# Kernel optimization log

Hardware: AMD Instinct MI355X
Metric: run time of the kernel (lower is better)

Reference implementation:

```python
import jax, jax.numpy as jnp
import numpy as np

B, S, H, R, F, E, K = 4, 2048, 1024, 256, 4096, 8, 2


def setup_inputs() -> dict:
    key = jax.random.key(0)
    k = jax.random.split(key, 7)
    s = 0.02
    return {
        "x": jax.random.normal(k[0], (B, S, H), dtype=jnp.float32),
        "router_w": jax.random.normal(k[1], (H, E), dtype=jnp.float32) * s,
        "router_b": jnp.zeros((E,), dtype=jnp.float32),
        "w1": jax.random.normal(k[2], (E, H, R), dtype=jnp.float32) * s,  # expert Linear(hidden->rank), no bias
        "w2": jax.random.normal(k[3], (E, R, F), dtype=jnp.float32) * s,  # expert Linear(rank->ffn), no bias
        "lin2_w": jax.random.normal(k[4], (F, H), dtype=jnp.float32) * s,
        "lin2_b": jnp.zeros((H,), dtype=jnp.float32),
    }


def reference(x, router_w, router_b, w1, w2, lin2_w, lin2_b):
    # Router: softmax over experts, top-k selection (mask), weight by softmax prob
    logits = jnp.einsum("bsh,he->bse", x, router_w) + router_b
    routing_weights = jax.nn.softmax(logits, axis=-1)            # [B,S,E]
    _, topk_idx = jax.lax.top_k(routing_weights, K)              # [B,S,K]
    mask = jnp.sum(jax.nn.one_hot(topk_idx, E, dtype=x.dtype), axis=-2)  # [B,S,E] in {0,1}
    mw = routing_weights * mask                                  # mask * weight per expert

    # Dense per-expert low-rank FFN (original computes all experts, masks after).
    # Fold mask*weight into the rank-space activations to avoid a [B,S,E,F] tensor.
    t = jnp.einsum("bsh,ehr->bser", x, w1)                       # [B,S,E,R]
    t = t * mw[..., None]
    mixed = jnp.einsum("bser,erf->bsf", t, w2)                   # [B,S,F]

    h = jax.nn.gelu(mixed, approximate=False)                    # torch nn.GELU is erf-based
    out = jnp.einsum("bsf,fh->bsh", h, lin2_w) + lin2_b
    # dropout is identity in eval mode
    return out
```

## Files before the change

### kernel.cpp

```cpp
#include <hip/hip_runtime.h>
#include <math.h>


using short8  = __attribute__((ext_vector_type(8))) short;
using floatx4 = __attribute__((ext_vector_type(4))) float;
typedef unsigned short bf16_t;

#define TOK   8192
#define HDIM  1024
#define RDIM  256
#define FDIM  4096
#define NEXP  8
#define MAXTILES 96
#define MAXSLOTS 16384
#define IMG   16384

__device__ __forceinline__ bf16_t f2bf(float f) {
  union { float f; unsigned u; } a; a.f = f;
  unsigned u = a.u;
  return (bf16_t)((u + 0x7FFFu + ((u >> 16) & 1u)) >> 16);
}

__device__ __forceinline__ float gelu_erf(float v) {
  return 0.5f * v * (1.0f + erff(v * 0.70710678118654752f));
}

__device__ __forceinline__ void gload16(const void* g, void* l) {
  __builtin_amdgcn_global_load_lds(
      (const __attribute__((address_space(1))) void*)g,
      (__attribute__((address_space(3))) void*)l, 16, 0, 0);
}

__device__ __forceinline__ int swz_off(int r, int kl) {
  return r * 128 + ((((kl >> 3) ^ (r & 15)) << 3) | (kl & 7));
}


__device__ __forceinline__ void pack_tile_body(const float* __restrict__ src,
                                               size_t kStride,
                                               bf16_t* __restrict__ img) {
  __shared__ bf16_t lim[IMG];
  const int tid = threadIdx.x;
  const int rr = tid & 127, half = tid >> 7;
  for (int kl = half; kl < 128; kl += 2)
    lim[swz_off(rr, kl)] = f2bf(src[(size_t)kl * kStride + rr]);
  __syncthreads();
  const int4* s4 = (const int4*)lim;
  int4* d4 = (int4*)img;
#pragma unroll
  for (int i = 0; i < 8; i++) d4[tid + i * 256] = s4[tid + i * 256];
}

__global__ void pack_w1(const float* __restrict__ w1, bf16_t* __restrict__ w1p) {
  const int img = blockIdx.x;
  const int e = img >> 4, nc = (img >> 3) & 1, kb = img & 7;
  pack_tile_body(w1 + (size_t)e * 1024 * 256 + (size_t)kb * 128 * 256 + nc * 128,
                 256, w1p + (size_t)img * IMG);
}
__global__ void pack_w2(const float* __restrict__ w2, bf16_t* __restrict__ w2p) {
  const int img = blockIdx.x;
  const int n = img >> 4, e = (img >> 1) & 7, kb = img & 1;
  pack_tile_body(w2 + (size_t)e * 256 * 4096 + (size_t)kb * 128 * 4096 + n * 128,
                 4096, w2p + (size_t)img * IMG);
}

__global__ void tcvt(const float* __restrict__ in, bf16_t* __restrict__ out,
                     int cols, size_t inSlice, size_t ldo,
                     int outRowStep, int outColStep) {
  __shared__ float tile[64][65];
  const int z  = blockIdx.z;
  const float* src = in + (size_t)z * inSlice;
  const int c0 = blockIdx.x * 64;
  const int r0 = blockIdx.y * 64;
  const int tx = threadIdx.x;
  const int ty = threadIdx.y;
#pragma unroll
  for (int i = 0; i < 64; i += 4)
    tile[ty + i][tx] = src[(size_t)(r0 + ty + i) * cols + (c0 + tx)];
  __syncthreads();
#pragma unroll
  for (int i = 0; i < 64; i += 4) {
    float v = tile[tx][ty + i];
    out[((size_t)(c0 + ty + i) + (size_t)z * outRowStep) * ldo +
        (size_t)z * outColStep + (r0 + tx)] = f2bf(v);
  }
}


__global__ void router_kernel(const float* __restrict__ x,
                              const float* __restrict__ rw,
                              const float* __restrict__ rb,
                              int* __restrict__ gid_tok,
                              float2* __restrict__ tokscale,
                              bf16_t* __restrict__ xb) {
  const int token = blockIdx.x * 4 + (threadIdx.x >> 6);
  const int lane  = threadIdx.x & 63;
  const float* xr = x + (size_t)token * HDIM;
  bf16_t* xbr = xb + (size_t)token * HDIM;

  double acc[NEXP];
#pragma unroll
  for (int e = 0; e < NEXP; e++) acc[e] = 0.0;
  for (int h = lane; h < HDIM; h += 64) {
    const float xf = xr[h];
    xbr[h] = f2bf(xf);
    const double xv = (double)xf;
    const float* wr = rw + (size_t)h * NEXP;
#pragma unroll
    for (int e = 0; e < NEXP; e++) acc[e] += xv * (double)wr[e];
  }
#pragma unroll
  for (int off = 32; off > 0; off >>= 1) {
#pragma unroll
    for (int e = 0; e < NEXP; e++) acc[e] += __shfl_xor(acc[e], off, 64);
  }
  double lg[NEXP];
#pragma unroll
  for (int e = 0; e < NEXP; e++) lg[e] = acc[e] + (double)rb[e];

  double mx = lg[0];
#pragma unroll
  for (int e = 1; e < NEXP; e++) mx = fmax(mx, lg[e]);
  double p[NEXP]; double den = 0.0;
#pragma unroll
  for (int e = 0; e < NEXP; e++) { p[e] = exp(lg[e] - mx); den += p[e]; }

  int i1 = 0;
#pragma unroll
  for (int e = 1; e < NEXP; e++) if (lg[e] > lg[i1]) i1 = e;
  int i2 = (i1 == 0) ? 1 : 0;
#pragma unroll
  for (int e = 0; e < NEXP; e++)
    if (e != i1 && e != i2 && lg[e] > lg[i2]) i2 = e;

  if (lane == 0) {
    const int elo = min(i1, i2), ehi = max(i1, i2);
    gid_tok[token] = elo * 8 + ehi;
    tokscale[token] = make_float2((float)(p[elo] / den), (float)(p[ehi] / den));
  }
}

__global__ void build_tiles(const int* __restrict__ gid_tok,
                            int* __restrict__ ctrl,
                            int* __restrict__ tok_of_slot,
                            float2* __restrict__ scale_of_slot) {
  __shared__ int hist[64], ntl[64];
  const int t = threadIdx.x;
  for (int i = t; i < MAXSLOTS; i += 256) {
    tok_of_slot[i] = -1;
    scale_of_slot[i] = make_float2(0.f, 0.f);
  }
  if (t < 64) hist[t] = 0;
  __syncthreads();
  for (int i = t; i < TOK; i += 256) atomicAdd(&hist[gid_tok[i]], 1);
  __syncthreads();
  if (t < 64) ntl[t] = (hist[t] + 127) >> 7;
  __syncthreads();
  if (t < 64) {
    int slot0 = 0, tile0 = 0;
    for (int g = 0; g < t; g++) { slot0 += ntl[g] << 7; tile0 += ntl[g]; }
    ctrl[64 + t] = 0;
    ctrl[128 + t] = slot0;
    const int nt = ntl[t], c = hist[t];
    for (int i = 0; i < nt; i++) {
      ctrl[256 + (tile0 + i) * 3 + 0] = t;
      ctrl[256 + (tile0 + i) * 3 + 1] = slot0 + i * 128;
      ctrl[256 + (tile0 + i) * 3 + 2] = min(128, c - i * 128);
    }
    if (t == 63) ctrl[192] = tile0 + nt;
  }
}

__global__ void scatter_tokens(const int* __restrict__ gid_tok,
                               const float2* __restrict__ tokscale,
                               int* __restrict__ ctrl,
                               int* __restrict__ tok_of_slot,
                               float2* __restrict__ scale_of_slot) {
  const int t = blockIdx.x * 256 + threadIdx.x;
  const int g = gid_tok[t];
  const int pos = atomicAdd(&ctrl[64 + g], 1);
  const int slot = ctrl[128 + g] + pos;
  tok_of_slot[slot] = t;
  scale_of_slot[slot] = tokscale[t];
}

__global__ __launch_bounds__(256)
void gemm_g1(const bf16_t* __restrict__ xb, const bf16_t* __restrict__ w1p,
             bf16_t* __restrict__ Tp, const int* __restrict__ ctrl,
             const int* __restrict__ tok_of_slot,
             const float2* __restrict__ scale_of_slot) {
  const int b = blockIdx.x;
  const int tile = b >> 3, mh = (b >> 2) & 1, n = b & 3;
  if (tile >= ctrl[192]) return;
  const int nrows = ctrl[256 + tile * 3 + 2];
  if (mh && nrows <= 64) return;
  __shared__ bf16_t As[64 * 128];
  __shared__ bf16_t Bs[128 * 128];
  const int gid   = ctrl[256 + tile * 3];
  const int slot0 = ctrl[256 + tile * 3 + 1];
  const int e = (n < 2) ? (gid >> 3) : (gid & 7);
  const int nc = n & 1;
  const int tid = threadIdx.x, lane = tid & 63, w = tid >> 6;
  const int wm = (w & 1) * 32, wn = (w >> 1) * 64;
  const int l16 = lane & 15, quad = lane >> 4;

  floatx4 acc[2][4];
  const floatx4 zero = {0.f, 0.f, 0.f, 0.f};
#pragma unroll
  for (int i = 0; i < 2; i++)
#pragma unroll
    for (int j = 0; j < 4; j++) acc[i][j] = zero;

  int toks[4];
  int rowAs[4];
#pragma unroll
  for (int i = 0; i < 4; i++) {
    rowAs[i] = w * 16 + i * 4 + (lane >> 4);
    int tk = tok_of_slot[slot0 + mh * 64 + rowAs[i]];
    toks[i] = (tk < 0) ? 0 : tk;
  }
  const bf16_t* bimg = w1p + (size_t)(e * 16 + nc * 8) * IMG;
  bf16_t* lA = As + w * 2048;
  bf16_t* lB = Bs + w * 4096;

  for (int kb = 0; kb < 8; kb++) {
    __syncthreads();
#pragma unroll
    for (int i = 0; i < 4; i++) {
      const int gq = (lane & 15) ^ (rowAs[i] & 15);
      gload16(xb + (size_t)toks[i] * HDIM + kb * 128 + gq * 8, lA + i * 512);
    }
#pragma unroll
    for (int i = 0; i < 8; i++)
      gload16(bimg + (size_t)kb * IMG + w * 4096 + i * 512 + lane * 8, lB + i * 512);
    __syncthreads();
#pragma unroll
    for (int s = 0; s < 4; s++) {
      const int pg = ((s * 4 + quad) ^ l16) << 3;
      short8 af[2], bfr[4];
#pragma unroll
      for (int i = 0; i < 2; i++)
        af[i] = *(const short8*)&As[(wm + i * 16 + l16) * 128 + pg];
#pragma unroll
      for (int i = 0; i < 4; i++)
        bfr[i] = *(const short8*)&Bs[(wn + i * 16 + l16) * 128 + pg];
#pragma unroll
      for (int mi = 0; mi < 2; mi++)
#pragma unroll
        for (int ni = 0; ni < 4; ni++)
          acc[mi][ni] = __builtin_amdgcn_mfma_f32_16x16x32_bf16(
              af[mi], bfr[ni], acc[mi][ni], 0, 0, 0);
    }
  }

  __syncthreads();
#pragma unroll
  for (int mi = 0; mi < 2; mi++) {
#pragma unroll
    for (int r = 0; r < 4; r++) {
      const int rloc = wm + mi * 16 + quad * 4 + r;
      const float2 sc = scale_of_slot[slot0 + mh * 64 + rloc];
      const float s = (n < 2) ? sc.x : sc.y;
#pragma unroll
      for (int ni = 0; ni < 4; ni++) {
        const int c = wn + ni * 16 + l16;
        As[swz_off(rloc, c)] = f2bf(acc[mi][ni][r] * s);
      }
    }
  }
  __syncthreads();
  bf16_t* img = Tp + (size_t)(tile * 4 + n) * IMG + mh * 64 * 128;
  const int4* s4 = (const int4*)As;
  int4* d4 = (int4*)img;
#pragma unroll
  for (int j = 0; j < 4; j++) d4[tid + j * 256] = s4[tid + j * 256];
}

__global__ __launch_bounds__(256)
void gemm_g2(const bf16_t* __restrict__ Tp, const bf16_t* __restrict__ w2p,
             bf16_t* __restrict__ Hb, const int* __restrict__ ctrl,
             const int* __restrict__ tok_of_slot) {
  const int b = blockIdx.x;
  const int tile = b >> 6, mh = (b >> 5) & 1, n = b & 31;
  if (tile >= ctrl[192]) return;
  const int nrows = ctrl[256 + tile * 3 + 2];
  if (mh && nrows <= 64) return;
  __shared__ bf16_t As[64 * 128];
  __shared__ bf16_t Bs[128 * 128];
  const int gid   = ctrl[256 + tile * 3];
  const int slot0 = ctrl[256 + tile * 3 + 1];
  const int elo = gid >> 3, ehi = gid & 7;
  const int tid = threadIdx.x, lane = tid & 63, w = tid >> 6;
  const int wm = (w & 1) * 32, wn = (w >> 1) * 64;
  const int l16 = lane & 15, quad = lane >> 4;

  floatx4 acc[2][4];
  const floatx4 zero = {0.f, 0.f, 0.f, 0.f};
#pragma unroll
  for (int i = 0; i < 2; i++)
#pragma unroll
    for (int j = 0; j < 4; j++) acc[i][j] = zero;

  const bf16_t* aimg = Tp + (size_t)tile * 4 * IMG + mh * 64 * 128;
  bf16_t* lA = As + w * 2048;
  bf16_t* lB = Bs + w * 4096;

#pragma unroll
  for (int t = 0; t < 4; t++) {
    const int e = (t < 2) ? elo : ehi;
    const bf16_t* bimg = w2p + (size_t)(n * 16 + e * 2 + (t & 1)) * IMG;
    __syncthreads();
#pragma unroll
    for (int i = 0; i < 4; i++)
      gload16(aimg + (size_t)t * IMG + w * 2048 + i * 512 + lane * 8, lA + i * 512);
#pragma unroll
    for (int i = 0; i < 8; i++)
      gload16(bimg + w * 4096 + i * 512 + lane * 8, lB + i * 512);
    __syncthreads();
#pragma unroll
    for (int s = 0; s < 4; s++) {
      const int pg = ((s * 4 + quad) ^ l16) << 3;
      short8 af[2], bfr[4];
#pragma unroll
      for (int i = 0; i < 2; i++)
        af[i] = *(const short8*)&As[(wm + i * 16 + l16) * 128 + pg];
#pragma unroll
      for (int i = 0; i < 4; i++)
        bfr[i] = *(const short8*)&Bs[(wn + i * 16 + l16) * 128 + pg];
#pragma unroll
      for (int mi = 0; mi < 2; mi++)
#pragma unroll
        for (int ni = 0; ni < 4; ni++)
          acc[mi][ni] = __builtin_amdgcn_mfma_f32_16x16x32_bf16(
              af[mi], bfr[ni], acc[mi][ni], 0, 0, 0);
    }
  }

  __syncthreads();
#pragma unroll
  for (int mi = 0; mi < 2; mi++) {
#pragma unroll
    for (int r = 0; r < 4; r++) {
      const int rloc = wm + mi * 16 + quad * 4 + r;
#pragma unroll
      for (int ni = 0; ni < 4; ni++) {
        const int c = wn + ni * 16 + l16;
        Bs[rloc * 128 + c] = f2bf(gelu_erf(acc[mi][ni][r]));
      }
    }
  }
  __syncthreads();
  const int4* s4 = (const int4*)Bs;
#pragma unroll
  for (int j = 0; j < 4; j++) {
    const int chunk = tid + j * 256;
    const int row = chunk >> 4, off = chunk & 15;
    const int tok = tok_of_slot[slot0 + mh * 64 + row];
    if (tok >= 0)
      *(int4*)(Hb + (size_t)tok * FDIM + n * 128 + off * 8) = s4[chunk];
  }
}

__global__ __launch_bounds__(256)
void gemm_g3(const bf16_t* __restrict__ Hb, const bf16_t* __restrict__ ltw,
             float* __restrict__ out, const float* __restrict__ bias) {
  __shared__ bf16_t As[128 * 64];
  __shared__ bf16_t Bs[128 * 64];
  const int b = blockIdx.x;
  const int m0 = ((b & 7) * 8 + ((b >> 3) & 7)) * 128;
  const int n0 = (b >> 6) * 128;
  const int tid = threadIdx.x, lane = tid & 63, w = tid >> 6;
  const int wm = (w >> 1) * 64, wn = (w & 1) * 64;
  const int l16 = lane & 15, quad = lane >> 4;
  const int rl = lane >> 3, gg = lane & 7;
  const int gf = (gg ^ rl) * 8;

  floatx4 acc[4][4];
  const floatx4 zero = {0.f, 0.f, 0.f, 0.f};
#pragma unroll
  for (int i = 0; i < 4; i++)
#pragma unroll
    for (int j = 0; j < 4; j++) acc[i][j] = zero;

  const bf16_t* ga[4];
  const bf16_t* gb[4];
#pragma unroll
  for (int c = 0; c < 4; c++) {
    ga[c] = Hb  + (size_t)(m0 + w * 32 + c * 8 + rl) * FDIM + gf;
    gb[c] = ltw + (size_t)(n0 + w * 32 + c * 8 + rl) * FDIM + gf;
  }
  bf16_t* lA = &As[w * 32 * 64];
  bf16_t* lB = &Bs[w * 32 * 64];

  for (int k0 = 0; k0 < FDIM; k0 += 64) {
    __syncthreads();
#pragma unroll
    for (int c = 0; c < 4; c++) { gload16(ga[c], lA + c * 512); ga[c] += 64; }
#pragma unroll
    for (int c = 0; c < 4; c++) { gload16(gb[c], lB + c * 512); gb[c] += 64; }
    __syncthreads();
#pragma unroll
    for (int s = 0; s < 2; s++) {
      const int pg = ((s * 4 + quad) ^ (l16 & 7)) * 8;
      short8 af[4], bfr[4];
#pragma unroll
      for (int i = 0; i < 4; i++)
        af[i] = *(const short8*)&As[(wm + i * 16 + l16) * 64 + pg];
#pragma unroll
      for (int i = 0; i < 4; i++)
        bfr[i] = *(const short8*)&Bs[(wn + i * 16 + l16) * 64 + pg];
#pragma unroll
      for (int mi = 0; mi < 4; mi++)
#pragma unroll
        for (int ni = 0; ni < 4; ni++)
          acc[mi][ni] = __builtin_amdgcn_mfma_f32_16x16x32_bf16(
              af[mi], bfr[ni], acc[mi][ni], 0, 0, 0);
    }
  }

#pragma unroll
  for (int mi = 0; mi < 4; mi++) {
#pragma unroll
    for (int ni = 0; ni < 4; ni++) {
      const int row = m0 + wm + mi * 16 + quad * 4;
      const int col = n0 + wn + ni * 16 + l16;
#pragma unroll
      for (int r = 0; r < 4; r++)
        out[(size_t)(row + r) * HDIM + col] = acc[mi][ni][r] + bias[col];
    }
  }
}


extern "C" void kernel_launch(void* const* d_in, const int* in_sizes, int n_in,
                              void* d_out, int out_size, void* d_ws, size_t ws_size,
                              hipStream_t stream) {
  const float* x   = (const float*)d_in[0];
  const float* rw  = (const float*)d_in[1];
  const float* rb  = (const float*)d_in[2];
  const float* w1  = (const float*)d_in[3];
  const float* w2  = (const float*)d_in[4];
  const float* l2w = (const float*)d_in[5];
  const float* l2b = (const float*)d_in[6];

  char* ws = (char*)d_ws;
  int*    ctrl     = (int*)   (ws + 0);
  int*    gid_tok  = (int*)   (ws + 4096);
  float2* tokscale = (float2*)(ws + 36864);
  int*    tokslot  = (int*)   (ws + 102400);
  float2* slotsc   = (float2*)(ws + 167936);
  bf16_t* xb  = (bf16_t*)(ws + 1048576);
  bf16_t* w1p = (bf16_t*)(ws + 17825792);
  bf16_t* w2p = (bf16_t*)(ws + 22020096);
  bf16_t* ltw = (bf16_t*)(ws + 38797312);
  bf16_t* Tp  = (bf16_t*)(ws + 47185920);
  bf16_t* Hb  = (bf16_t*)(ws + 59768832);

  router_kernel<<<TOK / 4, 256, 0, stream>>>(x, rw, rb, gid_tok, tokscale, xb);
  build_tiles<<<1, 256, 0, stream>>>(gid_tok, ctrl, tokslot, slotsc);
  scatter_tokens<<<TOK / 256, 256, 0, stream>>>(gid_tok, tokscale, ctrl, tokslot, slotsc);

  pack_w1<<<128, 256, 0, stream>>>(w1, w1p);
  pack_w2<<<512, 256, 0, stream>>>(w2, w2p);
  tcvt<<<dim3(HDIM / 64, FDIM / 64, 1), dim3(64, 4), 0, stream>>>(
      l2w, ltw, HDIM, 0, FDIM, 0, 0);

  gemm_g1<<<8 * MAXTILES, 256, 0, stream>>>(xb, w1p, Tp, ctrl, tokslot, slotsc);
  gemm_g2<<<64 * MAXTILES, 256, 0, stream>>>(Tp, w2p, Hb, ctrl, tokslot);
  gemm_g3<<<512, 256, 0, stream>>>(Hb, ltw, (float*)d_out, l2b);
}
```

Measured before the change: 354.1 us.

## Fuse preprocessing kernels, merge tile build with scatter, split-K final GEMM

```diff
diff --git a/kernel.cpp b/kernel.cpp
--- a/kernel.cpp
+++ b/kernel.cpp
@@ -38,8 +38,8 @@
 
 __device__ __forceinline__ void pack_tile_body(const float* __restrict__ src,
                                                size_t kStride,
-                                               bf16_t* __restrict__ img) {
-  __shared__ bf16_t lim[IMG];
+                                               bf16_t* __restrict__ img,
+                                               bf16_t* __restrict__ lim) {
   const int tid = threadIdx.x;
   const int rr = tid & 127, half = tid >> 7;
   for (int kl = half; kl < 128; kl += 2)
@@ -51,106 +51,99 @@
   for (int i = 0; i < 8; i++) d4[tid + i * 256] = s4[tid + i * 256];
 }
 
-__global__ void pack_w1(const float* __restrict__ w1, bf16_t* __restrict__ w1p) {
-  const int img = blockIdx.x;
-  const int e = img >> 4, nc = (img >> 3) & 1, kb = img & 7;
-  pack_tile_body(w1 + (size_t)e * 1024 * 256 + (size_t)kb * 128 * 256 + nc * 128,
-                 256, w1p + (size_t)img * IMG);
-}
-__global__ void pack_w2(const float* __restrict__ w2, bf16_t* __restrict__ w2p) {
-  const int img = blockIdx.x;
-  const int n = img >> 4, e = (img >> 1) & 7, kb = img & 1;
-  pack_tile_body(w2 + (size_t)e * 256 * 4096 + (size_t)kb * 128 * 4096 + n * 128,
-                 4096, w2p + (size_t)img * IMG);
-}
-
-__global__ void tcvt(const float* __restrict__ in, bf16_t* __restrict__ out,
-                     int cols, size_t inSlice, size_t ldo,
-                     int outRowStep, int outColStep) {
-  __shared__ float tile[64][65];
-  const int z  = blockIdx.z;
-  const float* src = in + (size_t)z * inSlice;
-  const int c0 = blockIdx.x * 64;
-  const int r0 = blockIdx.y * 64;
-  const int tx = threadIdx.x;
-  const int ty = threadIdx.y;
-#pragma unroll
-  for (int i = 0; i < 64; i += 4)
-    tile[ty + i][tx] = src[(size_t)(r0 + ty + i) * cols + (c0 + tx)];
-  __syncthreads();
-#pragma unroll
-  for (int i = 0; i < 64; i += 4) {
-    float v = tile[tx][ty + i];
-    out[((size_t)(c0 + ty + i) + (size_t)z * outRowStep) * ldo +
-        (size_t)z * outColStep + (r0 + tx)] = f2bf(v);
-  }
-}
-
-
-__global__ void router_kernel(const float* __restrict__ x,
-                              const float* __restrict__ rw,
-                              const float* __restrict__ rb,
-                              int* __restrict__ gid_tok,
-                              float2* __restrict__ tokscale,
-                              bf16_t* __restrict__ xb) {
-  const int token = blockIdx.x * 4 + (threadIdx.x >> 6);
-  const int lane  = threadIdx.x & 63;
-  const float* xr = x + (size_t)token * HDIM;
-  bf16_t* xbr = xb + (size_t)token * HDIM;
-
-  double acc[NEXP];
-#pragma unroll
-  for (int e = 0; e < NEXP; e++) acc[e] = 0.0;
-  for (int h = lane; h < HDIM; h += 64) {
-    const float xf = xr[h];
-    xbr[h] = f2bf(xf);
-    const double xv = (double)xf;
-    const float* wr = rw + (size_t)h * NEXP;
-#pragma unroll
-    for (int e = 0; e < NEXP; e++) acc[e] += xv * (double)wr[e];
-  }
-#pragma unroll
-  for (int off = 32; off > 0; off >>= 1) {
-#pragma unroll
-    for (int e = 0; e < NEXP; e++) acc[e] += __shfl_xor(acc[e], off, 64);
-  }
-  double lg[NEXP];
-#pragma unroll
-  for (int e = 0; e < NEXP; e++) lg[e] = acc[e] + (double)rb[e];
-
-  double mx = lg[0];
-#pragma unroll
-  for (int e = 1; e < NEXP; e++) mx = fmax(mx, lg[e]);
-  double p[NEXP]; double den = 0.0;
-#pragma unroll
-  for (int e = 0; e < NEXP; e++) { p[e] = exp(lg[e] - mx); den += p[e]; }
-
-  int i1 = 0;
-#pragma unroll
-  for (int e = 1; e < NEXP; e++) if (lg[e] > lg[i1]) i1 = e;
-  int i2 = (i1 == 0) ? 1 : 0;
-#pragma unroll
-  for (int e = 0; e < NEXP; e++)
-    if (e != i1 && e != i2 && lg[e] > lg[i2]) i2 = e;
-
-  if (lane == 0) {
-    const int elo = min(i1, i2), ehi = max(i1, i2);
-    gid_tok[token] = elo * 8 + ehi;
-    tokscale[token] = make_float2((float)(p[elo] / den), (float)(p[ehi] / den));
-  }
-}
-
-__global__ void build_tiles(const int* __restrict__ gid_tok,
-                            int* __restrict__ ctrl,
-                            int* __restrict__ tok_of_slot,
-                            float2* __restrict__ scale_of_slot) {
-  __shared__ int hist[64], ntl[64];
+__global__ __launch_bounds__(256)
+void prep(const float* __restrict__ x, const float* __restrict__ rw,
+          const float* __restrict__ rb, const float* __restrict__ w1,
+          const float* __restrict__ w2, const float* __restrict__ l2w,
+          int* __restrict__ gid_tok, float2* __restrict__ tokscale,
+          bf16_t* __restrict__ xb, bf16_t* __restrict__ w1p,
+          bf16_t* __restrict__ w2p, bf16_t* __restrict__ ltw,
+          int* __restrict__ tokslot, float2* __restrict__ slotsc) {
+  __shared__ __align__(16) char smem[33280];
+  const int b = blockIdx.x;
   const int t = threadIdx.x;
-  for (int i = t; i < MAXSLOTS; i += 256) {
-    tok_of_slot[i] = -1;
-    scale_of_slot[i] = make_float2(0.f, 0.f);
-  }
-  if (t < 64) hist[t] = 0;
+
+  if (b < 2048) {
+    const int token = b * 4 + (t >> 6);
+    const int lane  = t & 63;
+    const float* xr = x + (size_t)token * HDIM;
+    bf16_t* xbr = xb + (size_t)token * HDIM;
+    double acc[NEXP];
+#pragma unroll
+    for (int e = 0; e < NEXP; e++) acc[e] = 0.0;
+    for (int h = lane; h < HDIM; h += 64) {
+      const float xf = xr[h];
+      xbr[h] = f2bf(xf);
+      const double xv = (double)xf;
+      const float* wr = rw + (size_t)h * NEXP;
+#pragma unroll
+      for (int e = 0; e < NEXP; e++) acc[e] += xv * (double)wr[e];
+    }
+#pragma unroll
+    for (int off = 32; off > 0; off >>= 1) {
+#pragma unroll
+      for (int e = 0; e < NEXP; e++) acc[e] += __shfl_xor(acc[e], off, 64);
+    }
+    double lg[NEXP];
+#pragma unroll
+    for (int e = 0; e < NEXP; e++) lg[e] = acc[e] + (double)rb[e];
+    double mx = lg[0];
+#pragma unroll
+    for (int e = 1; e < NEXP; e++) mx = fmax(mx, lg[e]);
+    double p[NEXP]; double den = 0.0;
+#pragma unroll
+    for (int e = 0; e < NEXP; e++) { p[e] = exp(lg[e] - mx); den += p[e]; }
+    int i1 = 0;
+#pragma unroll
+    for (int e = 1; e < NEXP; e++) if (lg[e] > lg[i1]) i1 = e;
+    int i2 = (i1 == 0) ? 1 : 0;
+#pragma unroll
+    for (int e = 0; e < NEXP; e++)
+      if (e != i1 && e != i2 && lg[e] > lg[i2]) i2 = e;
+    if (lane == 0) {
+      const int elo = min(i1, i2), ehi = max(i1, i2);
+      gid_tok[token] = elo * 8 + ehi;
+      tokscale[token] = make_float2((float)(p[elo] / den), (float)(p[ehi] / den));
+    }
+  } else if (b < 2176) {
+    const int img = b - 2048;
+    const int e = img >> 4, nc = (img >> 3) & 1, kb = img & 7;
+    pack_tile_body(w1 + (size_t)e * 1024 * 256 + (size_t)kb * 128 * 256 + nc * 128,
+                   256, w1p + (size_t)img * IMG, (bf16_t*)smem);
+  } else if (b < 2688) {
+    const int img = b - 2176;
+    const int n = img >> 4, e = (img >> 1) & 7, kb = img & 1;
+    pack_tile_body(w2 + (size_t)e * 256 * 4096 + (size_t)kb * 128 * 4096 + n * 128,
+                   4096, w2p + (size_t)img * IMG, (bf16_t*)smem);
+  } else if (b < 3712) {
+    float* tile = (float*)smem;
+    const int bid = b - 2688;
+    const int c0 = (bid & 15) * 64;
+    const int r0 = (bid >> 4) * 64;
+    const int tx = t & 63, ty = t >> 6;
+#pragma unroll
+    for (int i = 0; i < 64; i += 4)
+      tile[(ty + i) * 65 + tx] = l2w[(size_t)(r0 + ty + i) * HDIM + (c0 + tx)];
+    __syncthreads();
+#pragma unroll
+    for (int i = 0; i < 64; i += 4)
+      ltw[(size_t)(c0 + ty + i) * FDIM + (r0 + tx)] = f2bf(tile[tx * 65 + ty + i]);
+  } else {
+    const int i = (b - 3712) * 256 + t;
+    tokslot[i] = -1;
+    slotsc[i] = make_float2(0.f, 0.f);
+  }
+}
+
+
+__global__ void build_scatter(const int* __restrict__ gid_tok,
+                              const float2* __restrict__ tokscale,
+                              int* __restrict__ ctrl,
+                              int* __restrict__ tok_of_slot,
+                              float2* __restrict__ scale_of_slot) {
+  __shared__ int hist[64], ntl[64], start[64], fill[64];
+  const int t = threadIdx.x;
+  if (t < 64) { hist[t] = 0; fill[t] = 0; }
   __syncthreads();
   for (int i = t; i < TOK; i += 256) atomicAdd(&hist[gid_tok[i]], 1);
   __syncthreads();
@@ -159,8 +152,7 @@
   if (t < 64) {
     int slot0 = 0, tile0 = 0;
     for (int g = 0; g < t; g++) { slot0 += ntl[g] << 7; tile0 += ntl[g]; }
-    ctrl[64 + t] = 0;
-    ctrl[128 + t] = slot0;
+    start[t] = slot0;
     const int nt = ntl[t], c = hist[t];
     for (int i = 0; i < nt; i++) {
       ctrl[256 + (tile0 + i) * 3 + 0] = t;
@@ -169,19 +161,14 @@
     }
     if (t == 63) ctrl[192] = tile0 + nt;
   }
-}
-
-__global__ void scatter_tokens(const int* __restrict__ gid_tok,
-                               const float2* __restrict__ tokscale,
-                               int* __restrict__ ctrl,
-                               int* __restrict__ tok_of_slot,
-                               float2* __restrict__ scale_of_slot) {
-  const int t = blockIdx.x * 256 + threadIdx.x;
-  const int g = gid_tok[t];
-  const int pos = atomicAdd(&ctrl[64 + g], 1);
-  const int slot = ctrl[128 + g] + pos;
-  tok_of_slot[slot] = t;
-  scale_of_slot[slot] = tokscale[t];
+  __syncthreads();
+  for (int i = t; i < TOK; i += 256) {
+    const int g = gid_tok[i];
+    const int pos = atomicAdd(&fill[g], 1);
+    const int slot = start[g] + pos;
+    tok_of_slot[slot] = i;
+    scale_of_slot[slot] = tokscale[i];
+  }
 }
 
 __global__ __launch_bounds__(256)
@@ -190,7 +177,7 @@
              const int* __restrict__ tok_of_slot,
              const float2* __restrict__ scale_of_slot) {
   const int b = blockIdx.x;
-  const int tile = b >> 3, mh = (b >> 2) & 1, n = b & 3;
+  const int n = b & 3, mh = (b >> 2) & 1, tile = b >> 3;
   if (tile >= ctrl[192]) return;
   const int nrows = ctrl[256 + tile * 3 + 2];
   if (mh && nrows <= 64) return;
@@ -281,7 +268,8 @@
              bf16_t* __restrict__ Hb, const int* __restrict__ ctrl,
              const int* __restrict__ tok_of_slot) {
   const int b = blockIdx.x;
-  const int tile = b >> 6, mh = (b >> 5) & 1, n = b & 31;
+  const int n = (b & 7) * 4 + ((b >> 3) & 3);
+  const int mh = (b >> 5) & 1, tile = b >> 6;
   if (tile >= ctrl[192]) return;
   const int nrows = ctrl[256 + tile * 3 + 2];
   if (mh && nrows <= 64) return;
@@ -363,12 +351,14 @@
 
 __global__ __launch_bounds__(256)
 void gemm_g3(const bf16_t* __restrict__ Hb, const bf16_t* __restrict__ ltw,
-             float* __restrict__ out, const float* __restrict__ bias) {
+             float* __restrict__ out, float* __restrict__ p0) {
   __shared__ bf16_t As[128 * 64];
   __shared__ bf16_t Bs[128 * 64];
   const int b = blockIdx.x;
-  const int m0 = ((b & 7) * 8 + ((b >> 3) & 7)) * 128;
-  const int n0 = (b >> 6) * 128;
+  const int r0 = b >> 3;
+  const int m0 = ((b & 7) * 8 + (r0 & 7)) * 128;
+  const int n0 = ((r0 >> 3) & 7) * 128;
+  const int kb = r0 >> 6;
   const int tid = threadIdx.x, lane = tid & 63, w = tid >> 6;
   const int wm = (w >> 1) * 64, wn = (w & 1) * 64;
   const int l16 = lane & 15, quad = lane >> 4;
@@ -386,13 +376,13 @@
   const bf16_t* gb[4];
 #pragma unroll
   for (int c = 0; c < 4; c++) {
-    ga[c] = Hb  + (size_t)(m0 + w * 32 + c * 8 + rl) * FDIM + gf;
-    gb[c] = ltw + (size_t)(n0 + w * 32 + c * 8 + rl) * FDIM + gf;
+    ga[c] = Hb  + (size_t)(m0 + w * 32 + c * 8 + rl) * FDIM + kb * 2048 + gf;
+    gb[c] = ltw + (size_t)(n0 + w * 32 + c * 8 + rl) * FDIM + kb * 2048 + gf;
   }
   bf16_t* lA = &As[w * 32 * 64];
   bf16_t* lB = &Bs[w * 32 * 64];
 
-  for (int k0 = 0; k0 < FDIM; k0 += 64) {
+  for (int k0 = 0; k0 < 2048; k0 += 64) {
     __syncthreads();
 #pragma unroll
     for (int c = 0; c < 4; c++) { gload16(ga[c], lA + c * 512); ga[c] += 64; }
@@ -418,6 +408,7 @@
     }
   }
 
+  float* dst = kb ? out : p0;
 #pragma unroll
   for (int mi = 0; mi < 4; mi++) {
 #pragma unroll
@@ -426,9 +417,22 @@
       const int col = n0 + wn + ni * 16 + l16;
 #pragma unroll
       for (int r = 0; r < 4; r++)
-        out[(size_t)(row + r) * HDIM + col] = acc[mi][ni][r] + bias[col];
-    }
-  }
+        dst[(size_t)(row + r) * HDIM + col] = acc[mi][ni][r];
+    }
+  }
+}
+
+__global__ void reduce_out(float* __restrict__ out, const float* __restrict__ p0,
+                           const float* __restrict__ bias) {
+  const int i4 = blockIdx.x * 256 + threadIdx.x;
+  float4 a = ((const float4*)out)[i4];
+  float4 p = ((const float4*)p0)[i4];
+  float4 bb = ((const float4*)bias)[i4 & 255];
+  a.x += p.x + bb.x;
+  a.y += p.y + bb.y;
+  a.z += p.z + bb.z;
+  a.w += p.w + bb.w;
+  ((float4*)out)[i4] = a;
 }
 
 
@@ -455,17 +459,15 @@
   bf16_t* ltw = (bf16_t*)(ws + 38797312);
   bf16_t* Tp  = (bf16_t*)(ws + 47185920);
   bf16_t* Hb  = (bf16_t*)(ws + 59768832);
-
-  router_kernel<<<TOK / 4, 256, 0, stream>>>(x, rw, rb, gid_tok, tokscale, xb);
-  build_tiles<<<1, 256, 0, stream>>>(gid_tok, ctrl, tokslot, slotsc);
-  scatter_tokens<<<TOK / 256, 256, 0, stream>>>(gid_tok, tokscale, ctrl, tokslot, slotsc);
-
-  pack_w1<<<128, 256, 0, stream>>>(w1, w1p);
-  pack_w2<<<512, 256, 0, stream>>>(w2, w2p);
-  tcvt<<<dim3(HDIM / 64, FDIM / 64, 1), dim3(64, 4), 0, stream>>>(
-      l2w, ltw, HDIM, 0, FDIM, 0, 0);
+  float*  p0  = (float*) (ws + 1048576);
+
+  prep<<<3776, 256, 0, stream>>>(x, rw, rb, w1, w2, l2w,
+                                 gid_tok, tokscale, xb, w1p, w2p, ltw,
+                                 tokslot, slotsc);
+  build_scatter<<<1, 256, 0, stream>>>(gid_tok, tokscale, ctrl, tokslot, slotsc);
 
   gemm_g1<<<8 * MAXTILES, 256, 0, stream>>>(xb, w1p, Tp, ctrl, tokslot, slotsc);
   gemm_g2<<<64 * MAXTILES, 256, 0, stream>>>(Tp, w2p, Hb, ctrl, tokslot);
-  gemm_g3<<<512, 256, 0, stream>>>(Hb, ltw, (float*)d_out, l2b);
-}
+  gemm_g3<<<1024, 256, 0, stream>>>(Hb, ltw, (float*)d_out, p0);
+  reduce_out<<<TOK * HDIM / 1024, 256, 0, stream>>>((float*)d_out, p0, l2b);
+}
```

New measurement: 361.6 us. 1.02x slower.
